# Performance work log

Hardware: AMD Instinct MI355X
Metric: run time of the kernel (lower is better)

## Reference

```python
import jax, jax.numpy as jnp
import numpy as np

# dims
B, LP, CIN, AUX = 8, 1024, 64, 32
COUT, OUT_LEN = 64, 512
DM, DI, NS, PH, NH = 1024, 2048, 16, 64, 32  # d_model, d_inner, d_state, headdim, n_heads
NL, PATCH, KPRE, KCONV = 4, 8, 5, 4
GG, KH, CHUNK = 8, 2048, 64  # kan grid, kan hidden, chunk_size
DIN = 2 * DI + 2 * NS + NH   # in_proj output: z, xBC, dt
CONV_DIM = DI + 2 * NS


def _conv1d(x, w, b, stride, pad_l, pad_r, groups=1):
    # x: [B, C, L], w: [O, I/groups, K]
    y = jax.lax.conv_general_dilated(x, w, (stride,), [(pad_l, pad_r)],
                                     dimension_numbers=("NCH", "OIH", "NCH"),
                                     feature_group_count=groups)
    return y + b[None, :, None]


def _rmsnorm(x, w):
    return x * jax.lax.rsqrt(jnp.mean(x * x, axis=-1, keepdims=True) + 1e-5) * w


def _mamba(u, in_w, conv_w, conv_b, A_log, Dh, dt_bias, out_w):
    # Mamba2-style selective SSM block (bias-free projections, causal depthwise conv).
    Bs, L, _ = u.shape
    zxbcdt = jnp.einsum("bld,ed->ble", u, in_w)  # [B,L,DIN]
    z = zxbcdt[..., :DI]
    xBC = zxbcdt[..., DI:DI + CONV_DIM]
    dt = jax.nn.softplus(zxbcdt[..., DI + CONV_DIM:] + dt_bias)  # [B,L,NH]
    xBC = jax.nn.silu(_conv1d(xBC.transpose(0, 2, 1), conv_w, conv_b, 1, KCONV - 1, 0,
                              groups=CONV_DIM)).transpose(0, 2, 1)
    xh = xBC[..., :DI].reshape(Bs, L, NH, PH)
    Bm = xBC[..., DI:DI + NS]   # [B,L,NS]
    Cm = xBC[..., DI + NS:]     # [B,L,NS]
    dA = jnp.exp(-jnp.exp(A_log) * dt)  # [B,L,NH]

    def step(s, t):
        x_t, B_t, C_t, dA_t, dt_t = t
        s = s * dA_t[:, :, None, None] + jnp.einsum("bhp,bn,bh->bhpn", x_t, B_t, dt_t)
        return s, jnp.einsum("bhpn,bn->bhp", s, C_t)

    s0 = jnp.zeros((Bs, NH, PH, NS), u.dtype)
    xs = (xh.transpose(1, 0, 2, 3), Bm.transpose(1, 0, 2), Cm.transpose(1, 0, 2),
          dA.transpose(1, 0, 2), dt.transpose(1, 0, 2))
    _, ys = jax.lax.scan(step, s0, xs)  # ys: [L,B,NH,PH]
    y = ys.transpose(1, 0, 2, 3) + xh * Dh[None, None, :, None]
    y = y.reshape(Bs, L, DI) * jax.nn.silu(z)
    return jnp.einsum("ble,de->bld", y, out_w)


def _kan(x, log_bw, base_w, base_b, spline_w):
    # Gaussian-basis KAN layer: base Linear + spline Linear over RBF expansion.
    grid = jnp.linspace(-2.0, 2.0, GG)
    bw = jnp.exp(log_bw)[None] + 1e-6                 # [1,in,1]
    basis = jnp.exp(-((x[..., None] - grid[None, None, :]) ** 2) / (2.0 * bw * bw))
    return x @ base_w.T + base_b + basis.reshape(x.shape[0], -1) @ spline_w.T


def setup_inputs() -> dict:
    ks = iter(jax.random.split(jax.random.key(0), 64))
    nrm = lambda shape, s=0.02: jax.random.normal(next(ks), shape, jnp.float32) * s
    inp = {"x_prefix": jax.random.normal(next(ks), (B, LP, CIN), jnp.float32),
           "y_aux": jax.random.normal(next(ks), (B, AUX), jnp.float32),
           "pre_conv_w": nrm((DM, CIN, KPRE), 0.1), "pre_conv_b": jnp.zeros((DM,)),
           "patch_w": nrm((DM, DM, PATCH), 0.05), "patch_b": jnp.zeros((DM,))}
    for pre in ("fwd", "bwd"):
        inp[pre + "_norm_w"] = jnp.ones((NL, DM))
        inp[pre + "_in_w"] = nrm((NL, DIN, DM))
        inp[pre + "_conv_w"] = nrm((NL, CONV_DIM, 1, KCONV), 0.1)
        inp[pre + "_conv_b"] = jnp.zeros((NL, CONV_DIM))
        inp[pre + "_A_log"] = jnp.zeros((NL, NH))
        inp[pre + "_D"] = jnp.ones((NL, NH))
        inp[pre + "_dt_bias"] = nrm((NL, NH), 0.5)
        inp[pre + "_out_w"] = nrm((NL, DM, DI))
    inp.update(aux_w=nrm((DM, AUX)), aux_b=jnp.zeros((DM,)),
               kan1_log_bw=jnp.zeros((3 * DM, 1)), kan1_base_w=nrm((KH, 3 * DM)),
               kan1_base_b=jnp.zeros((KH,)), kan1_spline_w=nrm((KH, 3 * DM * GG), 0.005),
               kan2_log_bw=jnp.zeros((KH, 1)), kan2_base_w=nrm((DM, KH)),
               kan2_base_b=jnp.zeros((DM,)), kan2_spline_w=nrm((DM, KH * GG), 0.005),
               shared_w=nrm((DM, DM)), shared_b=jnp.zeros((DM,)),
               heads_w=nrm((COUT, OUT_LEN, DM)), heads_b=jnp.zeros((COUT, OUT_LEN)))
    return inp


def reference(x_prefix, y_aux, pre_conv_w, pre_conv_b, patch_w, patch_b,
              fwd_norm_w, fwd_in_w, fwd_conv_w, fwd_conv_b, fwd_A_log, fwd_D, fwd_dt_bias, fwd_out_w,
              bwd_norm_w, bwd_in_w, bwd_conv_w, bwd_conv_b, bwd_A_log, bwd_D, bwd_dt_bias, bwd_out_w,
              aux_w, aux_b, kan1_log_bw, kan1_base_w, kan1_base_b, kan1_spline_w,
              kan2_log_bw, kan2_base_w, kan2_base_b, kan2_spline_w,
              shared_w, shared_b, heads_w, heads_b):
    # encode_prefix
    x = jax.nn.silu(_conv1d(x_prefix.transpose(0, 2, 1), pre_conv_w, pre_conv_b, 1, KPRE // 2, KPRE // 2))
    x = _conv1d(x, patch_w, patch_b, PATCH, 0, 0).transpose(0, 2, 1)  # [B, 128, DM]
    rem = x.shape[1] % CHUNK
    if rem:
        x = jnp.pad(x, ((0, 0), (0, CHUNK - rem), (0, 0)))
    h_f, h_b = x, x[:, ::-1]
    for i in range(NL):
        h_f = h_f + _mamba(_rmsnorm(h_f, fwd_norm_w[i]), fwd_in_w[i], fwd_conv_w[i], fwd_conv_b[i],
                           fwd_A_log[i], fwd_D[i], fwd_dt_bias[i], fwd_out_w[i])
        h_b = h_b + _mamba(_rmsnorm(h_b, bwd_norm_w[i]), bwd_in_w[i], bwd_conv_w[i], bwd_conv_b[i],
                           bwd_A_log[i], bwd_D[i], bwd_dt_bias[i], bwd_out_w[i])
    ctx = jnp.concatenate([h_f.mean(1), h_b[:, ::-1].mean(1)], axis=-1)  # [B, 2*DM]
    # fusion + heads
    aux = jax.nn.silu(y_aux @ aux_w.T + aux_b)
    fused = jnp.concatenate([ctx, aux], axis=-1)  # [B, 3*DM]
    fused = jax.nn.silu(_kan(fused, kan1_log_bw, kan1_base_w, kan1_base_b, kan1_spline_w))
    fused = jax.nn.silu(_kan(fused, kan2_log_bw, kan2_base_w, kan2_base_b, kan2_spline_w))
    fused = jax.nn.silu(fused @ shared_w.T + shared_b)
    # all channel heads fused into one batched GEMM: [B, OUT_LEN, COUT]
    return jnp.einsum("bd,cld->blc", fused, heads_w) + heads_b.T[None]
```

## Files before the change

### kernel.cpp

```cpp
#include <hip/hip_runtime.h>
#include <hip/hip_bf16.h>
#include <math.h>

#define B_    8
#define LP_   1024
#define CIN_  64
#define DM_   1024
#define DI_   2048
#define NS_   16
#define PH_   64
#define NH_   32
#define NL_   4
#define GG_   8
#define KH_   2048
#define DIN_  4160
#define NPAD_ 4224
#define CONVD_ 2080
#define L_    128
#define R_    1024
#define OUTL_ 512
#define COUT_ 64

typedef __bf16 bf16x8 __attribute__((ext_vector_type(8)));
typedef float f32x4 __attribute__((ext_vector_type(4)));
typedef unsigned short ushort;

__device__ __forceinline__ float silu_f(float x) { return x / (1.0f + expf(-x)); }

__device__ __forceinline__ ushort f2bu(float x) {
    union { __hip_bfloat16 h; ushort u; } c; c.h = __float2bfloat16(x); return c.u;
}
__device__ __forceinline__ float bu2f(ushort u) {
    union { ushort u; __hip_bfloat16 h; } c; c.u = u; return __bfloat162float(c.h);
}

__device__ __forceinline__ void gload_lds16(const void* g, void* l) {
    __builtin_amdgcn_global_load_lds((const __attribute__((address_space(1))) unsigned int*)g,
                                     (__attribute__((address_space(3))) unsigned int*)l, 16, 0, 0);
}

__device__ __forceinline__ float merge2(float a, float b, int mask, int lane) {
    float x = (lane & mask) ? b : a;
    float y = (lane & mask) ? a : b;
    return x + __shfl_xor(y, mask);
}
__device__ __forceinline__ float reduce8(float* a, int lane) {
    float c0 = merge2(a[0], a[1], 1, lane);
    float c1 = merge2(a[2], a[3], 1, lane);
    float c2 = merge2(a[4], a[5], 1, lane);
    float c3 = merge2(a[6], a[7], 1, lane);
    float d0 = merge2(c0, c1, 2, lane);
    float d1 = merge2(c2, c3, 2, lane);
    float e  = merge2(d0, d1, 4, lane);
    e += __shfl_xor(e, 8);
    e += __shfl_xor(e, 16);
    e += __shfl_xor(e, 32);
    return e;
}

__global__ __launch_bounds__(256) void k_pre_im2col(const float* __restrict__ xp, __hip_bfloat16* __restrict__ out) {
    size_t idx = (size_t)blockIdx.x * 256 + threadIdx.x;
    if (idx >= (size_t)8192 * 320) return;
    int kk = (int)(idx % 320); size_t r = idx / 320;
    int l = (int)(r & 1023); int b = (int)(r >> 10);
    int kp = kk >> 6, c = kk & 63;
    int lp = l + kp - 2;
    float v = 0.f;
    if (lp >= 0 && lp < LP_) v = xp[((size_t)b * LP_ + lp) * CIN_ + c];
    out[idx] = __float2bfloat16(v);
}

__global__ __launch_bounds__(256) void k_wpre_T(const float* __restrict__ w, __hip_bfloat16* __restrict__ out) {
    int idx = blockIdx.x * 256 + threadIdx.x;
    if (idx >= DM_ * 320) return;
    int d = idx / 320, kk = idx % 320;
    int kp = kk >> 6, c = kk & 63;
    out[idx] = __float2bfloat16(w[(d * CIN_ + c) * 5 + kp]);
}

__global__ __launch_bounds__(256) void k_wpatch_T(const float* __restrict__ w, __hip_bfloat16* __restrict__ out) {
    size_t idx = (size_t)blockIdx.x * 256 + threadIdx.x;
    if (idx >= (size_t)DM_ * 8192) return;
    int d = (int)(idx >> 13); int kk = (int)(idx & 8191);
    int kp = kk >> 10, din = kk & 1023;
    out[idx] = __float2bfloat16(w[((size_t)d << 13) + din * 8 + kp]);
}

#define CVT_IN_T4  1081344
#define CVT_OUT_T4 524288
__global__ __launch_bounds__(256) void k_cvt_layer(const float* __restrict__ in0, const float* __restrict__ in1,
                                                   const float* __restrict__ o0, const float* __restrict__ o1,
                                                   __hip_bfloat16* __restrict__ wBB, __hip_bfloat16* __restrict__ wOB) {
    int i = blockIdx.x * 256 + threadIdx.x;
    int dir = 0;
    if (i >= CVT_IN_T4 + CVT_OUT_T4) { dir = 1; i -= CVT_IN_T4 + CVT_OUT_T4; }
    const float* inw = dir ? in1 : in0;
    const float* outw = dir ? o1 : o0;
    if (i < CVT_IN_T4) {
        int idx = i * 4; int row = idx >> 10;
        __hip_bfloat16* dst = wBB + (size_t)dir * NPAD_ * 1024 + idx;
        if (row < DIN_) {
            float4 v = *(const float4*)(inw + idx);
            dst[0] = __float2bfloat16(v.x); dst[1] = __float2bfloat16(v.y);
            dst[2] = __float2bfloat16(v.z); dst[3] = __float2bfloat16(v.w);
        } else {
            dst[0] = __float2bfloat16(0.f); dst[1] = __float2bfloat16(0.f);
            dst[2] = __float2bfloat16(0.f); dst[3] = __float2bfloat16(0.f);
        }
    } else {
        int idx = (i - CVT_IN_T4) * 4;
        __hip_bfloat16* dst = wOB + (size_t)dir * 1024 * 2048 + idx;
        float4 v = *(const float4*)(outw + idx);
        dst[0] = __float2bfloat16(v.x); dst[1] = __float2bfloat16(v.y);
        dst[2] = __float2bfloat16(v.z); dst[3] = __float2bfloat16(v.w);
    }
}

template<int BM, int BN>
__global__ __launch_bounds__(256) void k_gemm_mfma(
    const ushort* __restrict__ A, const ushort* __restrict__ B,
    const float* __restrict__ bias,
    float* __restrict__ Cf, __hip_bfloat16* __restrict__ Cb,
    int Kc, int ldk, int ldc, int Nstore, int act, int nsplit,
    long sA, long sB, long sC)
{
    constexpr int BK = 32;
    constexpr int WM = BM / 2, WN = BN / 2;
    constexpr int MR = WM / 16, NR = WN / 16;
    constexpr int ACH = BM * 4, BCH = BN * 4;
    __shared__ ushort sAs[2][BM * BK];
    __shared__ ushort sBs[2][BN * BK];
    int tid = threadIdx.x;
    int lane = tid & 63, w = tid >> 6;
    int wr = w >> 1, wc = w & 1;
    int z = blockIdx.z;
    int dir = z / nsplit, ks = z - dir * nsplit;
    int kbase = ks * Kc;
    int m0 = blockIdx.y * BM, n0 = blockIdx.x * BN;
    const ushort* Az = A + (size_t)dir * sA + kbase;
    const ushort* Bz = B + (size_t)dir * sB + kbase;

    auto STAGE = [&](int buf, int k0) {
        #pragma unroll
        for (int c = tid; c < ACH; c += 256) {
            int row = c >> 2, col = (c & 3) * 8;
            gload_lds16(Az + (size_t)(m0 + row) * ldk + k0 + col, (char*)&sAs[buf][0] + c * 16);
        }
        #pragma unroll
        for (int c = tid; c < BCH; c += 256) {
            int row = c >> 2, col = (c & 3) * 8;
            gload_lds16(Bz + (size_t)(n0 + row) * ldk + k0 + col, (char*)&sBs[buf][0] + c * 16);
        }
    };

    f32x4 acc[MR][NR] = {};
    const int NT = Kc / BK;
    STAGE(0, 0);
    __syncthreads();
    int cur = 0;
    for (int t = 0; t < NT; ++t) {
        if (t + 1 < NT) STAGE(cur ^ 1, (t + 1) * BK);
        bf16x8 af[MR], bfr[NR];
        #pragma unroll
        for (int m = 0; m < MR; ++m)
            af[m] = *(const bf16x8*)&sAs[cur][(wr * WM + m * 16 + (lane & 15)) * BK + (lane >> 4) * 8];
        #pragma unroll
        for (int n = 0; n < NR; ++n)
            bfr[n] = *(const bf16x8*)&sBs[cur][(wc * WN + n * 16 + (lane & 15)) * BK + (lane >> 4) * 8];
        #pragma unroll
        for (int m = 0; m < MR; ++m)
            #pragma unroll
            for (int n = 0; n < NR; ++n)
                acc[m][n] = __builtin_amdgcn_mfma_f32_16x16x32_bf16(af[m], bfr[n], acc[m][n], 0, 0, 0);
        __syncthreads();
        cur ^= 1;
    }
    #pragma unroll
    for (int m = 0; m < MR; ++m) {
        int row = m0 + wr * WM + m * 16 + (lane >> 4) * 4;
        #pragma unroll
        for (int n = 0; n < NR; ++n) {
            int col = n0 + wc * WN + n * 16 + (lane & 15);
            if (col < Nstore) {
                if (act == 2) {
                    float* Cfz = Cf + (size_t)z * sC;
                    #pragma unroll
                    for (int j = 0; j < 4; ++j)
                        Cfz[(size_t)(row + j) * ldc + col] = acc[m][n][j];
                } else {
                    __hip_bfloat16* Cbz = Cb + (size_t)dir * sC;
                    float bv = bias ? bias[col] : 0.f;
                    #pragma unroll
                    for (int j = 0; j < 4; ++j) {
                        float v = acc[m][n][j] + bv;
                        if (act == 1) v = silu_f(v);
                        Cbz[(size_t)(row + j) * ldc + col] = __float2bfloat16(v);
                    }
                }
            }
        }
    }
}

__global__ __launch_bounds__(256) void k_patch_fin(const float* __restrict__ part, const float* __restrict__ bias,
                                                   float* __restrict__ hf, float* __restrict__ hb) {
    int i4 = blockIdx.x * 256 + threadIdx.x;
    int idx = i4 * 4;
    int r = idx >> 10, c = idx & 1023;
    float4 bv = *(const float4*)(bias + c);
    float4 o = bv;
    #pragma unroll
    for (int s = 0; s < 8; ++s) {
        float4 v = *(const float4*)(part + (size_t)s * 1048576 + idx);
        o.x += v.x; o.y += v.y; o.z += v.z; o.w += v.w;
    }
    *(float4*)(hf + idx) = o;
    *(float4*)(hb + (((size_t)(r ^ 127)) << 10) + c) = o;
}

__global__ __launch_bounds__(256) void k_oproj_fin(const float* __restrict__ part, float* __restrict__ h) {
    int i4 = blockIdx.x * 256 + threadIdx.x;
    int idx = i4 * 4;
    int dir = idx >> 20;
    int off = idx & 1048575;
    const float* p = part + (size_t)dir * 4 * 1048576 + off;
    float4 o = *(const float4*)(h + idx);
    #pragma unroll
    for (int s = 0; s < 4; ++s) {
        float4 v = *(const float4*)(p + (size_t)s * 1048576);
        o.x += v.x; o.y += v.y; o.z += v.z; o.w += v.w;
    }
    *(float4*)(h + idx) = o;
}

__global__ __launch_bounds__(256) void k_rmsnorm(const float* __restrict__ h, const float* __restrict__ w0,
                                                 const float* __restrict__ w1, __hip_bfloat16* __restrict__ u) {
    int r = blockIdx.x; int t = threadIdx.x;
    const float* w = (r >> 10) ? w1 : w0;
    const float* row = h + (size_t)r * DM_;
    float v[4]; float ss = 0.f;
    #pragma unroll
    for (int i = 0; i < 4; ++i) { v[i] = row[t + 256 * i]; ss += v[i] * v[i]; }
    #pragma unroll
    for (int o = 32; o; o >>= 1) ss += __shfl_xor(ss, o);
    __shared__ float sred[4];
    if ((t & 63) == 0) sred[t >> 6] = ss;
    __syncthreads();
    float tot = sred[0] + sred[1] + sred[2] + sred[3];
    float scale = rsqrtf(tot * (1.0f / DM_) + 1e-5f);
    #pragma unroll
    for (int i = 0; i < 4; ++i)
        u[(size_t)r * DM_ + t + 256 * i] = __float2bfloat16(v[i] * scale * w[t + 256 * i]);
}

__global__ __launch_bounds__(256) void k_scan(const __hip_bfloat16* __restrict__ zx,
                                              const float* __restrict__ cw0, const float* __restrict__ cw1,
                                              const float* __restrict__ cb0, const float* __restrict__ cb1,
                                              const float* __restrict__ dtb0, const float* __restrict__ dtb1,
                                              const float* __restrict__ al0, const float* __restrict__ al1,
                                              const float* __restrict__ D0, const float* __restrict__ D1,
                                              __hip_bfloat16* __restrict__ ys) {
    __shared__ float xs[L_ * PH_];
    __shared__ float Bsh[L_ * NS_];
    __shared__ float Csh[L_ * NS_];
    __shared__ float dts[L_];
    __shared__ float dAs[L_];
    int bx = blockIdx.x;
    int dir = bx >> 8, b = (bx >> 5) & 7, h = bx & 31;
    const __hip_bfloat16* zxd = zx + (size_t)dir * 1024 * DIN_;
    const float* cw = dir ? cw1 : cw0;
    const float* cb = dir ? cb1 : cb0;
    const float* dt_bias = dir ? dtb1 : dtb0;
    const float* A_log   = dir ? al1 : al0;
    const float* Dh      = dir ? D1 : D0;
    __hip_bfloat16* ysd  = ys + (size_t)dir * 1024 * DI_;
    int t = threadIdx.x;
    for (int i = t; i < 2048; i += 256) {
        int l = i >> 4, p4 = i & 15;
        int cc = h * PH_ + p4 * 4;
        float a0 = cb[cc + 0], a1 = cb[cc + 1], a2 = cb[cc + 2], a3 = cb[cc + 3];
        #pragma unroll
        for (int k = 0; k < 4; ++k) {
            int lp = l - 3 + k;
            if (lp >= 0) {
                ushort4 raw = *(const ushort4*)(zxd + (size_t)(b * L_ + lp) * DIN_ + DI_ + cc);
                a0 += bu2f(raw.x) * cw[(cc + 0) * 4 + k];
                a1 += bu2f(raw.y) * cw[(cc + 1) * 4 + k];
                a2 += bu2f(raw.z) * cw[(cc + 2) * 4 + k];
                a3 += bu2f(raw.w) * cw[(cc + 3) * 4 + k];
            }
        }
        float* xp = &xs[l * PH_ + p4 * 4];
        xp[0] = silu_f(a0); xp[1] = silu_f(a1); xp[2] = silu_f(a2); xp[3] = silu_f(a3);
    }
    for (int i = t; i < 1024; i += 256) {
        int l = i >> 3, q4 = i & 7;
        int cc = DI_ + q4 * 4;
        float a0 = cb[cc + 0], a1 = cb[cc + 1], a2 = cb[cc + 2], a3 = cb[cc + 3];
        #pragma unroll
        for (int k = 0; k < 4; ++k) {
            int lp = l - 3 + k;
            if (lp >= 0) {
                ushort4 raw = *(const ushort4*)(zxd + (size_t)(b * L_ + lp) * DIN_ + DI_ + cc);
                a0 += bu2f(raw.x) * cw[(cc + 0) * 4 + k];
                a1 += bu2f(raw.y) * cw[(cc + 1) * 4 + k];
                a2 += bu2f(raw.z) * cw[(cc + 2) * 4 + k];
                a3 += bu2f(raw.w) * cw[(cc + 3) * 4 + k];
            }
        }
        float r0 = silu_f(a0), r1 = silu_f(a1), r2 = silu_f(a2), r3 = silu_f(a3);
        if (q4 < 4) {
            float* bp = &Bsh[l * NS_ + q4 * 4];
            bp[0] = r0; bp[1] = r1; bp[2] = r2; bp[3] = r3;
        } else {
            float* cp = &Csh[l * NS_ + (q4 - 4) * 4];
            cp[0] = r0; cp[1] = r1; cp[2] = r2; cp[3] = r3;
        }
    }
    if (t < L_) {
        float v = bu2f(*(const ushort*)(zxd + (size_t)(b * L_ + t) * DIN_ + 4128 + h)) + dt_bias[h];
        float sp = v > 20.f ? v : log1pf(expf(v));
        dts[t] = sp;
        dAs[t] = expf(-expf(A_log[h]) * sp);
    }
    __syncthreads();
    int p = t >> 2, n0 = (t & 3) * 4;
    float Dv = Dh[h];
    float s0 = 0.f, s1 = 0.f, s2 = 0.f, s3 = 0.f;
    for (int l = 0; l < L_; ++l) {
        float x = xs[l * 64 + p];
        float dAv = dAs[l];
        float xdt = x * dts[l];
        s0 = s0 * dAv + xdt * Bsh[l * 16 + n0 + 0];
        s1 = s1 * dAv + xdt * Bsh[l * 16 + n0 + 1];
        s2 = s2 * dAv + xdt * Bsh[l * 16 + n0 + 2];
        s3 = s3 * dAv + xdt * Bsh[l * 16 + n0 + 3];
        float cp = s0 * Csh[l * 16 + n0 + 0] + s1 * Csh[l * 16 + n0 + 1]
                 + s2 * Csh[l * 16 + n0 + 2] + s3 * Csh[l * 16 + n0 + 3];
        cp += __shfl_xor(cp, 1);
        cp += __shfl_xor(cp, 2);
        if ((t & 3) == 0) xs[l * 64 + p] = cp + x * Dv;
    }
    __syncthreads();
    for (int i = t; i < L_ * PH_; i += 256) {
        int l = i >> 6, pp = i & 63;
        float z = bu2f(*(const ushort*)(zxd + (size_t)(b * L_ + l) * DIN_ + h * PH_ + pp));
        ysd[((size_t)(b * L_ + l)) * DI_ + h * PH_ + pp] = __float2bfloat16(xs[i] * silu_f(z));
    }
}

__global__ __launch_bounds__(256) void k_meanctx(const float* __restrict__ hf, const float* __restrict__ hb,
                                                 float* __restrict__ fused) {
    int b = blockIdx.x >> 3, ch = blockIdx.x & 7;
    int t = threadIdx.x;
    int d4 = t & 31, lg = t >> 5;
    int d = ch * 128 + d4 * 4;
    float4 sf = {0,0,0,0}, sb = {0,0,0,0};
    for (int l = lg; l < L_; l += 8) {
        float4 a = *(const float4*)(hf + ((size_t)b * L_ + l) * DM_ + d);
        float4 c = *(const float4*)(hb + ((size_t)b * L_ + l) * DM_ + d);
        sf.x += a.x; sf.y += a.y; sf.z += a.z; sf.w += a.w;
        sb.x += c.x; sb.y += c.y; sb.z += c.z; sb.w += c.w;
    }
    __shared__ float rf[8][128], rb[8][128];
    *(float4*)&rf[lg][d4 * 4] = sf;
    *(float4*)&rb[lg][d4 * 4] = sb;
    __syncthreads();
    if (t < 128) {
        float s1 = 0.f, s2 = 0.f;
        #pragma unroll
        for (int g = 0; g < 8; ++g) { s1 += rf[g][t]; s2 += rb[g][t]; }
        fused[b * 3072 + ch * 128 + t] = s1 * (1.f / L_);
        fused[b * 3072 + DM_ + ch * 128 + t] = s2 * (1.f / L_);
    }
}

__global__ __launch_bounds__(256) void k_aux(const float* __restrict__ y_aux, const float* __restrict__ aux_w,
                                             const float* __restrict__ aux_b, float* __restrict__ fused) {
    int j = blockIdx.x * 256 + threadIdx.x;
    if (j >= DM_) return;
    for (int b = 0; b < B_; ++b) {
        float acc = aux_b[j];
        for (int a = 0; a < 32; ++a) acc += y_aux[b * 32 + a] * aux_w[j * 32 + a];
        fused[b * 3072 + 2 * DM_ + j] = silu_f(acc);
    }
}

__global__ __launch_bounds__(256) void k_basis(const float* __restrict__ x, const float* __restrict__ log_bw,
                                               float* __restrict__ basis, int Din) {
    int idx = blockIdx.x * 256 + threadIdx.x;
    if (idx >= 8 * Din) return;
    int d = idx % Din;
    float xv = x[idx];
    float bw = expf(log_bw[d]) + 1e-6f;
    float inv = 1.0f / (2.0f * bw * bw);
    #pragma unroll
    for (int g = 0; g < GG_; ++g) {
        float gg = -2.0f + g * (4.0f / 7.0f);
        float df = xv - gg;
        basis[(size_t)idx * GG_ + g] = expf(-df * df * inv);
    }
}

template<int MODE>
__global__ __launch_bounds__(256) void k_dotl(const float* __restrict__ W, const float* __restrict__ X,
                                              const float* __restrict__ bias, float* __restrict__ out,
                                              int K, int Dout, int ldx, int nch, int chOff) {
    __shared__ float sX[8][1024];
    int ch = blockIdx.y;
    int k0 = ch * 1024;
    int tid = threadIdx.x;
    for (int i = tid; i < 2048; i += 256) {
        int b = i >> 8, kk = (i & 255) * 4;
        *(float4*)&sX[b][kk] = *(const float4*)(X + (size_t)b * ldx + k0 + kk);
    }
    __syncthreads();
    int wv = tid >> 6, lane = tid & 63;
    int rowBase = blockIdx.x * 32 + wv * 8;
    for (int j = 0; j < 8; ++j) {
        int row = rowBase + j;
        const float* wr = W + (size_t)row * K + k0;
        float acc[8] = {};
        #pragma unroll
        for (int it = 0; it < 4; ++it) {
            int k = it * 256 + lane * 4;
            float4 wvv = *(const float4*)(wr + k);
            #pragma unroll
            for (int b = 0; b < 8; ++b) {
                float4 xv = *(const float4*)&sX[b][k];
                acc[b] += wvv.x * xv.x + wvv.y * xv.y + wvv.z * xv.z + wvv.w * xv.w;
            }
        }
        float e = reduce8(acc, lane);
        if (lane < 8) {
            if (MODE == 0) {
                out[((size_t)row * nch + chOff + ch) * 8 + lane] = e;
            } else if (MODE == 1) {
                out[(size_t)lane * Dout + row] = silu_f(e + bias[row]);
            } else {
                int c = row >> 9, l = row & 511;
                out[((size_t)lane * OUTL_ + l) * COUT_ + c] = e + bias[row];
            }
        }
    }
}

template<int NCH>
__global__ __launch_bounds__(256) void k_dot_fin(const float* __restrict__ partial, const float* __restrict__ base_b,
                                                 float* __restrict__ out, int Dout) {
    int row = blockIdx.x * 256 + threadIdx.x;
    if (row >= Dout) return;
    float bb = base_b[row];
    #pragma unroll
    for (int b = 0; b < 8; ++b) {
        float s = bb;
        #pragma unroll
        for (int c = 0; c < NCH; ++c) s += partial[((size_t)row * NCH + c) * 8 + b];
        out[(size_t)b * Dout + row] = silu_f(s);
    }
}

extern "C" void kernel_launch(void* const* d_in, const int* in_sizes, int n_in,
                              void* d_out, int out_size, void* d_ws, size_t ws_size,
                              hipStream_t stream) {
    const float* x_prefix = (const float*)d_in[0];
    const float* y_aux    = (const float*)d_in[1];
    const float* pre_w    = (const float*)d_in[2];
    const float* pre_b    = (const float*)d_in[3];
    const float* patch_w  = (const float*)d_in[4];
    const float* patch_b  = (const float*)d_in[5];
    const float* norm_w[2] = {(const float*)d_in[6],  (const float*)d_in[14]};
    const float* in_w[2]   = {(const float*)d_in[7],  (const float*)d_in[15]};
    const float* conv_w[2] = {(const float*)d_in[8],  (const float*)d_in[16]};
    const float* conv_b[2] = {(const float*)d_in[9],  (const float*)d_in[17]};
    const float* A_log[2]  = {(const float*)d_in[10], (const float*)d_in[18]};
    const float* Dvec[2]   = {(const float*)d_in[11], (const float*)d_in[19]};
    const float* dt_b[2]   = {(const float*)d_in[12], (const float*)d_in[20]};
    const float* out_w[2]  = {(const float*)d_in[13], (const float*)d_in[21]};
    const float* aux_w = (const float*)d_in[22];
    const float* aux_b = (const float*)d_in[23];
    const float* k1_lbw = (const float*)d_in[24];
    const float* k1_bw  = (const float*)d_in[25];
    const float* k1_bb  = (const float*)d_in[26];
    const float* k1_sw  = (const float*)d_in[27];
    const float* k2_lbw = (const float*)d_in[28];
    const float* k2_bw  = (const float*)d_in[29];
    const float* k2_bb  = (const float*)d_in[30];
    const float* k2_sw  = (const float*)d_in[31];
    const float* sh_w = (const float*)d_in[32];
    const float* sh_b = (const float*)d_in[33];
    const float* hw   = (const float*)d_in[34];
    const float* hbias= (const float*)d_in[35];
    float* ws = (float*)d_ws;
    float* out = (float*)d_out;

    const size_t o_ApreB   = 0;
    const size_t o_wpreTB  = 1310720;
    const size_t o_x1B     = 1474560;
    const size_t o_wpatchTB= 5668864;
    const size_t o_uB   = 0;
    const size_t o_zxB  = 1048576;
    const size_t o_ysB  = 5308416;
    const size_t o_wBB  = 7405568;
    const size_t o_wOB  = 11730944;
    const size_t o_hf   = 13828096;
    const size_t o_hb   = 14876672;
    const size_t o_spart= 15925248;
    const size_t total_f = 24313856;
    const size_t o_f1   = 0;
    const size_t o_bas1 = 24576;
    const size_t o_k1   = 221184;
    const size_t o_bas2 = 237568;
    const size_t o_k2   = 368640;
    const size_t o_f4   = 376832;
    const size_t o_part = 385024;
    if (ws_size < total_f * sizeof(float)) return;

    __hip_bfloat16* ApreB   = (__hip_bfloat16*)(ws + o_ApreB);
    __hip_bfloat16* wpreTB  = (__hip_bfloat16*)(ws + o_wpreTB);
    __hip_bfloat16* x1B     = (__hip_bfloat16*)(ws + o_x1B);
    __hip_bfloat16* wpatchTB= (__hip_bfloat16*)(ws + o_wpatchTB);
    __hip_bfloat16* uB      = (__hip_bfloat16*)(ws + o_uB);
    __hip_bfloat16* zxB     = (__hip_bfloat16*)(ws + o_zxB);
    __hip_bfloat16* ysB     = (__hip_bfloat16*)(ws + o_ysB);
    __hip_bfloat16* wBB     = (__hip_bfloat16*)(ws + o_wBB);
    __hip_bfloat16* wOB     = (__hip_bfloat16*)(ws + o_wOB);
    float* hf = ws + o_hf;
    float* hb = ws + o_hb;

    k_wpre_T<<<1280, 256, 0, stream>>>(pre_w, wpreTB);
    k_wpatch_T<<<32768, 256, 0, stream>>>(patch_w, wpatchTB);
    k_pre_im2col<<<10240, 256, 0, stream>>>(x_prefix, ApreB);
    k_gemm_mfma<128,128><<<dim3(8, 64, 1), 256, 0, stream>>>(
        (const ushort*)ApreB, (const ushort*)wpreTB, pre_b, nullptr, x1B,
        320, 320, 1024, 1024, 1, 1, 0, 0, 0);
    k_gemm_mfma<128,128><<<dim3(8, 8, 8), 256, 0, stream>>>(
        (const ushort*)x1B, (const ushort*)wpatchTB, nullptr, ws + o_spart, nullptr,
        1024, 8192, 1024, 1024, 2, 8, 0, 0, (long)1024 * 1024);
    k_patch_fin<<<1024, 256, 0, stream>>>(ws + o_spart, patch_b, hf, hb);

    for (int i = 0; i < NL_; ++i) {
        k_rmsnorm<<<2048, 256, 0, stream>>>(hf, norm_w[0] + (size_t)i * DM_, norm_w[1] + (size_t)i * DM_, uB);
        k_cvt_layer<<<12544, 256, 0, stream>>>(
            in_w[0] + (size_t)i * DIN_ * DM_, in_w[1] + (size_t)i * DIN_ * DM_,
            out_w[0] + (size_t)i * DM_ * DI_, out_w[1] + (size_t)i * DM_ * DI_, wBB, wOB);
        k_gemm_mfma<128,128><<<dim3(33, 8, 2), 256, 0, stream>>>(
            (const ushort*)uB, (const ushort*)wBB, nullptr, nullptr, zxB,
            1024, 1024, DIN_, DIN_, 0, 1, (long)1024 * 1024, (long)NPAD_ * 1024, (long)1024 * DIN_);
        k_scan<<<512, 256, 0, stream>>>(zxB,
            conv_w[0] + (size_t)i * CONVD_ * 4, conv_w[1] + (size_t)i * CONVD_ * 4,
            conv_b[0] + (size_t)i * CONVD_, conv_b[1] + (size_t)i * CONVD_,
            dt_b[0] + i * NH_, dt_b[1] + i * NH_, A_log[0] + i * NH_, A_log[1] + i * NH_,
            Dvec[0] + i * NH_, Dvec[1] + i * NH_, ysB);
        k_gemm_mfma<128,128><<<dim3(8, 8, 8), 256, 0, stream>>>(
            (const ushort*)ysB, (const ushort*)wOB, nullptr, ws + o_spart, nullptr,
            512, 2048, 1024, 1024, 2, 4, (long)1024 * 2048, (long)1024 * 2048, (long)1024 * 1024);
        k_oproj_fin<<<2048, 256, 0, stream>>>(ws + o_spart, hf);
    }

    k_meanctx<<<64, 256, 0, stream>>>(hf, hb, ws + o_f1);
    k_aux<<<4, 256, 0, stream>>>(y_aux, aux_w, aux_b, ws + o_f1);
    k_basis<<<96, 256, 0, stream>>>(ws + o_f1, k1_lbw, ws + o_bas1, 3072);
    k_dotl<0><<<dim3(64, 24), 256, 0, stream>>>(k1_sw, ws + o_bas1, nullptr, ws + o_part, 24576, 2048, 24576, 27, 0);
    k_dotl<0><<<dim3(64, 3),  256, 0, stream>>>(k1_bw, ws + o_f1,   nullptr, ws + o_part, 3072,  2048, 3072,  27, 24);
    k_dot_fin<27><<<8, 256, 0, stream>>>(ws + o_part, k1_bb, ws + o_k1, 2048);
    k_basis<<<64, 256, 0, stream>>>(ws + o_k1, k2_lbw, ws + o_bas2, 2048);
    k_dotl<0><<<dim3(32, 16), 256, 0, stream>>>(k2_sw, ws + o_bas2, nullptr, ws + o_part, 16384, 1024, 16384, 18, 0);
    k_dotl<0><<<dim3(32, 2),  256, 0, stream>>>(k2_bw, ws + o_k1,   nullptr, ws + o_part, 2048,  1024, 2048,  18, 16);
    k_dot_fin<18><<<4, 256, 0, stream>>>(ws + o_part, k2_bb, ws + o_k2, 1024);
    k_dotl<1><<<dim3(32, 1), 256, 0, stream>>>(sh_w, ws + o_k2, sh_b, ws + o_f4, 1024, 1024, 1024, 1, 0);
    k_dotl<2><<<dim3(1024, 1), 256, 0, stream>>>(hw, ws + o_f4, hbias, out, 1024, 32768, 1024, 1, 0);
}
```

Before: 918.7 us.

## Fuse small kernels and convert all layer weights up front in one launch

Merges the three preprocessing kernels into one launch, and converts all layers' weights to bf16 in a single kernel before the layer loop instead of once per layer. The residual-add finish kernels now also compute the next layer's RMSNorm, and the mean/aux, KAN spline/base dot, and finish+basis kernels are merged. The aim is to cut kernel launch count and extra passes over the activations, at the cost of a much larger workspace holding all converted weights.

Measured after the change: 883.0 us. -3.9%, faster.

```diff
diff --git a/kernel.cpp b/kernel.cpp
--- a/kernel.cpp
+++ b/kernel.cpp
@@ -58,47 +58,51 @@
     return e;
 }
 
-__global__ __launch_bounds__(256) void k_pre_im2col(const float* __restrict__ xp, __hip_bfloat16* __restrict__ out) {
-    size_t idx = (size_t)blockIdx.x * 256 + threadIdx.x;
-    if (idx >= (size_t)8192 * 320) return;
-    int kk = (int)(idx % 320); size_t r = idx / 320;
-    int l = (int)(r & 1023); int b = (int)(r >> 10);
-    int kp = kk >> 6, c = kk & 63;
-    int lp = l + kp - 2;
-    float v = 0.f;
-    if (lp >= 0 && lp < LP_) v = xp[((size_t)b * LP_ + lp) * CIN_ + c];
-    out[idx] = __float2bfloat16(v);
-}
-
-__global__ __launch_bounds__(256) void k_wpre_T(const float* __restrict__ w, __hip_bfloat16* __restrict__ out) {
+#define PREP_W1 327680
+#define PREP_W2 8388608
+#define PREP_W3 2621440
+__global__ __launch_bounds__(256) void k_prep(const float* __restrict__ pre_w, const float* __restrict__ patch_w,
+                                              const float* __restrict__ xp,
+                                              __hip_bfloat16* __restrict__ wpreT, __hip_bfloat16* __restrict__ wpatchT,
+                                              __hip_bfloat16* __restrict__ Apre) {
     int idx = blockIdx.x * 256 + threadIdx.x;
-    if (idx >= DM_ * 320) return;
-    int d = idx / 320, kk = idx % 320;
-    int kp = kk >> 6, c = kk & 63;
-    out[idx] = __float2bfloat16(w[(d * CIN_ + c) * 5 + kp]);
-}
-
-__global__ __launch_bounds__(256) void k_wpatch_T(const float* __restrict__ w, __hip_bfloat16* __restrict__ out) {
-    size_t idx = (size_t)blockIdx.x * 256 + threadIdx.x;
-    if (idx >= (size_t)DM_ * 8192) return;
-    int d = (int)(idx >> 13); int kk = (int)(idx & 8191);
-    int kp = kk >> 10, din = kk & 1023;
-    out[idx] = __float2bfloat16(w[((size_t)d << 13) + din * 8 + kp]);
+    if (idx < PREP_W1) {
+        int d = idx / 320, kk = idx % 320;
+        int kp = kk >> 6, c = kk & 63;
+        wpreT[idx] = __float2bfloat16(pre_w[(d * CIN_ + c) * 5 + kp]);
+    } else if (idx < PREP_W1 + PREP_W2) {
+        int i = idx - PREP_W1;
+        int d = i >> 13, kk = i & 8191;
+        int kp = kk >> 10, din = kk & 1023;
+        wpatchT[i] = __float2bfloat16(patch_w[((size_t)d << 13) + din * 8 + kp]);
+    } else if (idx < PREP_W1 + PREP_W2 + PREP_W3) {
+        int i = idx - PREP_W1 - PREP_W2;
+        int kk = i % 320; int r = i / 320;
+        int l = r & 1023, b = r >> 10;
+        int kp = kk >> 6, c = kk & 63;
+        int lp = l + kp - 2;
+        float v = 0.f;
+        if (lp >= 0 && lp < LP_) v = xp[((size_t)b * LP_ + lp) * CIN_ + c];
+        Apre[i] = __float2bfloat16(v);
+    }
 }
 
 #define CVT_IN_T4  1081344
 #define CVT_OUT_T4 524288
-__global__ __launch_bounds__(256) void k_cvt_layer(const float* __restrict__ in0, const float* __restrict__ in1,
-                                                   const float* __restrict__ o0, const float* __restrict__ o1,
-                                                   __hip_bfloat16* __restrict__ wBB, __hip_bfloat16* __restrict__ wOB) {
+#define CVT_PER    1605632
+__global__ __launch_bounds__(256) void k_cvt_all(const float* __restrict__ in0, const float* __restrict__ in1,
+                                                 const float* __restrict__ o0, const float* __restrict__ o1,
+                                                 __hip_bfloat16* __restrict__ wBBa, __hip_bfloat16* __restrict__ wOBa) {
     int i = blockIdx.x * 256 + threadIdx.x;
-    int dir = 0;
-    if (i >= CVT_IN_T4 + CVT_OUT_T4) { dir = 1; i -= CVT_IN_T4 + CVT_OUT_T4; }
-    const float* inw = dir ? in1 : in0;
-    const float* outw = dir ? o1 : o0;
-    if (i < CVT_IN_T4) {
-        int idx = i * 4; int row = idx >> 10;
-        __hip_bfloat16* dst = wBB + (size_t)dir * NPAD_ * 1024 + idx;
+    if (i >= 8 * CVT_PER) return;
+    int ld = i / CVT_PER;
+    int r = i - ld * CVT_PER;
+    int l = ld >> 1, d = ld & 1;
+    const float* inw  = (d ? in1 : in0) + (size_t)l * DIN_ * DM_;
+    const float* outw = (d ? o1 : o0) + (size_t)l * DM_ * DI_;
+    if (r < CVT_IN_T4) {
+        int idx = r * 4; int row = idx >> 10;
+        __hip_bfloat16* dst = wBBa + (size_t)ld * NPAD_ * 1024 + idx;
         if (row < DIN_) {
             float4 v = *(const float4*)(inw + idx);
             dst[0] = __float2bfloat16(v.x); dst[1] = __float2bfloat16(v.y);
@@ -108,8 +112,8 @@
             dst[2] = __float2bfloat16(0.f); dst[3] = __float2bfloat16(0.f);
         }
     } else {
-        int idx = (i - CVT_IN_T4) * 4;
-        __hip_bfloat16* dst = wOB + (size_t)dir * 1024 * 2048 + idx;
+        int idx = (r - CVT_IN_T4) * 4;
+        __hip_bfloat16* dst = wOBa + (size_t)ld * 2048 * 1024 + idx;
         float4 v = *(const float4*)(outw + idx);
         dst[0] = __float2bfloat16(v.x); dst[1] = __float2bfloat16(v.y);
         dst[2] = __float2bfloat16(v.z); dst[3] = __float2bfloat16(v.w);
@@ -202,55 +206,70 @@
     }
 }
 
-__global__ __launch_bounds__(256) void k_patch_fin(const float* __restrict__ part, const float* __restrict__ bias,
-                                                   float* __restrict__ hf, float* __restrict__ hb) {
-    int i4 = blockIdx.x * 256 + threadIdx.x;
-    int idx = i4 * 4;
-    int r = idx >> 10, c = idx & 1023;
-    float4 bv = *(const float4*)(bias + c);
-    float4 o = bv;
+__global__ __launch_bounds__(256) void k_patch_fin_rms(const float* __restrict__ part, const float* __restrict__ bias,
+                                                       const float* __restrict__ w0, const float* __restrict__ w1,
+                                                       float* __restrict__ hf, float* __restrict__ hb,
+                                                       __hip_bfloat16* __restrict__ uB) {
+    int r = blockIdx.x;
+    int t = threadIdx.x;
+    int c = t * 4;
+    float4 o = *(const float4*)(bias + c);
     #pragma unroll
     for (int s = 0; s < 8; ++s) {
-        float4 v = *(const float4*)(part + (size_t)s * 1048576 + idx);
+        float4 v = *(const float4*)(part + (size_t)s * 1048576 + ((size_t)r << 10) + c);
         o.x += v.x; o.y += v.y; o.z += v.z; o.w += v.w;
     }
-    *(float4*)(hf + idx) = o;
-    *(float4*)(hb + (((size_t)(r ^ 127)) << 10) + c) = o;
-}
-
-__global__ __launch_bounds__(256) void k_oproj_fin(const float* __restrict__ part, float* __restrict__ h) {
-    int i4 = blockIdx.x * 256 + threadIdx.x;
-    int idx = i4 * 4;
-    int dir = idx >> 20;
-    int off = idx & 1048575;
-    const float* p = part + (size_t)dir * 4 * 1048576 + off;
-    float4 o = *(const float4*)(h + idx);
+    *(float4*)(hf + ((size_t)r << 10) + c) = o;
+    int rb = r ^ 127;
+    *(float4*)(hb + ((size_t)rb << 10) + c) = o;
+    float ss = o.x * o.x + o.y * o.y + o.z * o.z + o.w * o.w;
     #pragma unroll
-    for (int s = 0; s < 4; ++s) {
-        float4 v = *(const float4*)(p + (size_t)s * 1048576);
-        o.x += v.x; o.y += v.y; o.z += v.z; o.w += v.w;
-    }
-    *(float4*)(h + idx) = o;
-}
-
-__global__ __launch_bounds__(256) void k_rmsnorm(const float* __restrict__ h, const float* __restrict__ w0,
-                                                 const float* __restrict__ w1, __hip_bfloat16* __restrict__ u) {
-    int r = blockIdx.x; int t = threadIdx.x;
-    const float* w = (r >> 10) ? w1 : w0;
-    const float* row = h + (size_t)r * DM_;
-    float v[4]; float ss = 0.f;
-    #pragma unroll
-    for (int i = 0; i < 4; ++i) { v[i] = row[t + 256 * i]; ss += v[i] * v[i]; }
-    #pragma unroll
-    for (int o = 32; o; o >>= 1) ss += __shfl_xor(ss, o);
+    for (int of = 32; of; of >>= 1) ss += __shfl_xor(ss, of);
     __shared__ float sred[4];
     if ((t & 63) == 0) sred[t >> 6] = ss;
     __syncthreads();
     float tot = sred[0] + sred[1] + sred[2] + sred[3];
     float scale = rsqrtf(tot * (1.0f / DM_) + 1e-5f);
+    float4 wf = *(const float4*)(w0 + c);
+    float4 wb = *(const float4*)(w1 + c);
+    __hip_bfloat16* uf = uB + ((size_t)r << 10) + c;
+    __hip_bfloat16* ub = uB + ((size_t)(1024 + rb) << 10) + c;
+    uf[0] = __float2bfloat16(o.x * scale * wf.x); uf[1] = __float2bfloat16(o.y * scale * wf.y);
+    uf[2] = __float2bfloat16(o.z * scale * wf.z); uf[3] = __float2bfloat16(o.w * scale * wf.w);
+    ub[0] = __float2bfloat16(o.x * scale * wb.x); ub[1] = __float2bfloat16(o.y * scale * wb.y);
+    ub[2] = __float2bfloat16(o.z * scale * wb.z); ub[3] = __float2bfloat16(o.w * scale * wb.w);
+}
+
+template<bool DO_RMS>
+__global__ __launch_bounds__(256) void k_oproj_fin_rms(const float* __restrict__ part,
+                                                       const float* __restrict__ w0, const float* __restrict__ w1,
+                                                       float* __restrict__ h, __hip_bfloat16* __restrict__ uB) {
+    int row = blockIdx.x;
+    int t = threadIdx.x;
+    int c = t * 4;
+    const float* p = part + (size_t)(row >> 10) * 4194304 + (size_t)(row & 1023) * 1024 + c;
+    float4 o = *(const float4*)(h + ((size_t)row << 10) + c);
     #pragma unroll
-    for (int i = 0; i < 4; ++i)
-        u[(size_t)r * DM_ + t + 256 * i] = __float2bfloat16(v[i] * scale * w[t + 256 * i]);
+    for (int s = 0; s < 4; ++s) {
+        float4 v = *(const float4*)(p + (size_t)s * 1048576);
+        o.x += v.x; o.y += v.y; o.z += v.z; o.w += v.w;
+    }
+    *(float4*)(h + ((size_t)row << 10) + c) = o;
+    if (DO_RMS) {
+        float ss = o.x * o.x + o.y * o.y + o.z * o.z + o.w * o.w;
+        #pragma unroll
+        for (int of = 32; of; of >>= 1) ss += __shfl_xor(ss, of);
+        __shared__ float sred[4];
+        if ((t & 63) == 0) sred[t >> 6] = ss;
+        __syncthreads();
+        float tot = sred[0] + sred[1] + sred[2] + sred[3];
+        float scale = rsqrtf(tot * (1.0f / DM_) + 1e-5f);
+        const float* w = (row >> 10) ? w1 : w0;
+        float4 wv = *(const float4*)(w + c);
+        __hip_bfloat16* u = uB + ((size_t)row << 10) + c;
+        u[0] = __float2bfloat16(o.x * scale * wv.x); u[1] = __float2bfloat16(o.y * scale * wv.y);
+        u[2] = __float2bfloat16(o.z * scale * wv.z); u[3] = __float2bfloat16(o.w * scale * wv.w);
+    }
 }
 
 __global__ __launch_bounds__(256) void k_scan(const __hip_bfloat16* __restrict__ zx,
@@ -349,40 +368,41 @@
     }
 }
 
-__global__ __launch_bounds__(256) void k_meanctx(const float* __restrict__ hf, const float* __restrict__ hb,
-                                                 float* __restrict__ fused) {
-    int b = blockIdx.x >> 3, ch = blockIdx.x & 7;
+__global__ __launch_bounds__(256) void k_meanctx_aux(const float* __restrict__ hf, const float* __restrict__ hb,
+                                                     const float* __restrict__ y_aux, const float* __restrict__ aux_w,
+                                                     const float* __restrict__ aux_b, float* __restrict__ fused) {
+    int bx = blockIdx.x;
     int t = threadIdx.x;
-    int d4 = t & 31, lg = t >> 5;
-    int d = ch * 128 + d4 * 4;
-    float4 sf = {0,0,0,0}, sb = {0,0,0,0};
-    for (int l = lg; l < L_; l += 8) {
-        float4 a = *(const float4*)(hf + ((size_t)b * L_ + l) * DM_ + d);
-        float4 c = *(const float4*)(hb + ((size_t)b * L_ + l) * DM_ + d);
-        sf.x += a.x; sf.y += a.y; sf.z += a.z; sf.w += a.w;
-        sb.x += c.x; sb.y += c.y; sb.z += c.z; sb.w += c.w;
-    }
-    __shared__ float rf[8][128], rb[8][128];
-    *(float4*)&rf[lg][d4 * 4] = sf;
-    *(float4*)&rb[lg][d4 * 4] = sb;
-    __syncthreads();
-    if (t < 128) {
-        float s1 = 0.f, s2 = 0.f;
-        #pragma unroll
-        for (int g = 0; g < 8; ++g) { s1 += rf[g][t]; s2 += rb[g][t]; }
-        fused[b * 3072 + ch * 128 + t] = s1 * (1.f / L_);
-        fused[b * 3072 + DM_ + ch * 128 + t] = s2 * (1.f / L_);
-    }
-}
-
-__global__ __launch_bounds__(256) void k_aux(const float* __restrict__ y_aux, const float* __restrict__ aux_w,
-                                             const float* __restrict__ aux_b, float* __restrict__ fused) {
-    int j = blockIdx.x * 256 + threadIdx.x;
-    if (j >= DM_) return;
-    for (int b = 0; b < B_; ++b) {
-        float acc = aux_b[j];
-        for (int a = 0; a < 32; ++a) acc += y_aux[b * 32 + a] * aux_w[j * 32 + a];
-        fused[b * 3072 + 2 * DM_ + j] = silu_f(acc);
+    if (bx < 64) {
+        int b = bx >> 3, ch = bx & 7;
+        int d4 = t & 31, lg = t >> 5;
+        int d = ch * 128 + d4 * 4;
+        float4 sf = {0,0,0,0}, sb = {0,0,0,0};
+        for (int l = lg; l < L_; l += 8) {
+            float4 a = *(const float4*)(hf + ((size_t)b * L_ + l) * DM_ + d);
+            float4 c = *(const float4*)(hb + ((size_t)b * L_ + l) * DM_ + d);
+            sf.x += a.x; sf.y += a.y; sf.z += a.z; sf.w += a.w;
+            sb.x += c.x; sb.y += c.y; sb.z += c.z; sb.w += c.w;
+        }
+        __shared__ float rf[8][128], rb[8][128];
+        *(float4*)&rf[lg][d4 * 4] = sf;
+        *(float4*)&rb[lg][d4 * 4] = sb;
+        __syncthreads();
+        if (t < 128) {
+            float s1 = 0.f, s2 = 0.f;
+            #pragma unroll
+            for (int g = 0; g < 8; ++g) { s1 += rf[g][t]; s2 += rb[g][t]; }
+            fused[b * 3072 + ch * 128 + t] = s1 * (1.f / L_);
+            fused[b * 3072 + DM_ + ch * 128 + t] = s2 * (1.f / L_);
+        }
+    } else {
+        int j = (bx - 64) * 256 + t;
+        if (j >= DM_) return;
+        for (int b = 0; b < B_; ++b) {
+            float acc = aux_b[j];
+            for (int a = 0; a < 32; ++a) acc += y_aux[b * 32 + a] * aux_w[j * 32 + a];
+            fused[b * 3072 + 2 * DM_ + j] = silu_f(acc);
+        }
     }
 }
 
@@ -403,16 +423,21 @@
 }
 
 template<int MODE>
-__global__ __launch_bounds__(256) void k_dotl(const float* __restrict__ W, const float* __restrict__ X,
+__global__ __launch_bounds__(256) void k_dotk(const float* __restrict__ Wsp, const float* __restrict__ Xsp, int Ksp,
+                                              const float* __restrict__ Wb, const float* __restrict__ Xb, int Kb,
                                               const float* __restrict__ bias, float* __restrict__ out,
-                                              int K, int Dout, int ldx, int nch, int chOff) {
+                                              int nsp, int nch, int Dout) {
     __shared__ float sX[8][1024];
     int ch = blockIdx.y;
-    int k0 = ch * 1024;
+    bool sp = (ch < nsp);
+    const float* W = sp ? Wsp : Wb;
+    const float* X = sp ? Xsp : Xb;
+    int K = sp ? Ksp : Kb;
+    int k0 = (sp ? ch : ch - nsp) * 1024;
     int tid = threadIdx.x;
     for (int i = tid; i < 2048; i += 256) {
         int b = i >> 8, kk = (i & 255) * 4;
-        *(float4*)&sX[b][kk] = *(const float4*)(X + (size_t)b * ldx + k0 + kk);
+        *(float4*)&sX[b][kk] = *(const float4*)(X + (size_t)b * K + k0 + kk);
     }
     __syncthreads();
     int wv = tid >> 6, lane = tid & 63;
@@ -434,13 +459,37 @@
         float e = reduce8(acc, lane);
         if (lane < 8) {
             if (MODE == 0) {
-                out[((size_t)row * nch + chOff + ch) * 8 + lane] = e;
+                out[((size_t)row * nch + ch) * 8 + lane] = e;
             } else if (MODE == 1) {
                 out[(size_t)lane * Dout + row] = silu_f(e + bias[row]);
             } else {
                 int c = row >> 9, l = row & 511;
                 out[((size_t)lane * OUTL_ + l) * COUT_ + c] = e + bias[row];
             }
+        }
+    }
+}
+
+__global__ __launch_bounds__(256) void k_fin1_basis2(const float* __restrict__ partial, const float* __restrict__ bb,
+                                                     const float* __restrict__ k2_lbw,
+                                                     float* __restrict__ k1, float* __restrict__ bas2) {
+    int row = blockIdx.x * 256 + threadIdx.x;
+    if (row >= 2048) return;
+    float bbv = bb[row];
+    float lb = expf(k2_lbw[row]) + 1e-6f;
+    float inv = 1.0f / (2.0f * lb * lb);
+    #pragma unroll
+    for (int b = 0; b < 8; ++b) {
+        float s = bbv;
+        #pragma unroll
+        for (int c = 0; c < 27; ++c) s += partial[((size_t)row * 27 + c) * 8 + b];
+        float v = silu_f(s);
+        k1[(size_t)b * 2048 + row] = v;
+        #pragma unroll
+        for (int g = 0; g < GG_; ++g) {
+            float gg = -2.0f + g * (4.0f / 7.0f);
+            float df = v - gg;
+            bas2[((size_t)b * 2048 + row) * GG_ + g] = expf(-df * df * inv);
         }
     }
 }
@@ -501,12 +550,12 @@
     const size_t o_uB   = 0;
     const size_t o_zxB  = 1048576;
     const size_t o_ysB  = 5308416;
-    const size_t o_wBB  = 7405568;
-    const size_t o_wOB  = 11730944;
-    const size_t o_hf   = 13828096;
-    const size_t o_hb   = 14876672;
-    const size_t o_spart= 15925248;
-    const size_t total_f = 24313856;
+    const size_t o_hf   = 9863168;
+    const size_t o_hb   = 10911744;
+    const size_t o_wBBa = 11960320;
+    const size_t o_wOBa = 29261824;
+    const size_t o_spart= 37650432;
+    const size_t total_f = 46039040;
     const size_t o_f1   = 0;
     const size_t o_bas1 = 24576;
     const size_t o_k1   = 221184;
@@ -523,29 +572,24 @@
     __hip_bfloat16* uB      = (__hip_bfloat16*)(ws + o_uB);
     __hip_bfloat16* zxB     = (__hip_bfloat16*)(ws + o_zxB);
     __hip_bfloat16* ysB     = (__hip_bfloat16*)(ws + o_ysB);
-    __hip_bfloat16* wBB     = (__hip_bfloat16*)(ws + o_wBB);
-    __hip_bfloat16* wOB     = (__hip_bfloat16*)(ws + o_wOB);
+    __hip_bfloat16* wBBa    = (__hip_bfloat16*)(ws + o_wBBa);
+    __hip_bfloat16* wOBa    = (__hip_bfloat16*)(ws + o_wOBa);
     float* hf = ws + o_hf;
     float* hb = ws + o_hb;
 
-    k_wpre_T<<<1280, 256, 0, stream>>>(pre_w, wpreTB);
-    k_wpatch_T<<<32768, 256, 0, stream>>>(patch_w, wpatchTB);
-    k_pre_im2col<<<10240, 256, 0, stream>>>(x_prefix, ApreB);
+    k_cvt_all<<<50176, 256, 0, stream>>>(in_w[0], in_w[1], out_w[0], out_w[1], wBBa, wOBa);
+    k_prep<<<44288, 256, 0, stream>>>(pre_w, patch_w, x_prefix, wpreTB, wpatchTB, ApreB);
     k_gemm_mfma<128,128><<<dim3(8, 64, 1), 256, 0, stream>>>(
         (const ushort*)ApreB, (const ushort*)wpreTB, pre_b, nullptr, x1B,
         320, 320, 1024, 1024, 1, 1, 0, 0, 0);
     k_gemm_mfma<128,128><<<dim3(8, 8, 8), 256, 0, stream>>>(
         (const ushort*)x1B, (const ushort*)wpatchTB, nullptr, ws + o_spart, nullptr,
         1024, 8192, 1024, 1024, 2, 8, 0, 0, (long)1024 * 1024);
-    k_patch_fin<<<1024, 256, 0, stream>>>(ws + o_spart, patch_b, hf, hb);
+    k_patch_fin_rms<<<1024, 256, 0, stream>>>(ws + o_spart, patch_b, norm_w[0], norm_w[1], hf, hb, uB);
 
     for (int i = 0; i < NL_; ++i) {
-        k_rmsnorm<<<2048, 256, 0, stream>>>(hf, norm_w[0] + (size_t)i * DM_, norm_w[1] + (size_t)i * DM_, uB);
-        k_cvt_layer<<<12544, 256, 0, stream>>>(
-            in_w[0] + (size_t)i * DIN_ * DM_, in_w[1] + (size_t)i * DIN_ * DM_,
-            out_w[0] + (size_t)i * DM_ * DI_, out_w[1] + (size_t)i * DM_ * DI_, wBB, wOB);
         k_gemm_mfma<128,128><<<dim3(33, 8, 2), 256, 0, stream>>>(
-            (const ushort*)uB, (const ushort*)wBB, nullptr, nullptr, zxB,
+            (const ushort*)uB, (const ushort*)(wBBa + (size_t)i * 2 * NPAD_ * 1024), nullptr, nullptr, zxB,
             1024, 1024, DIN_, DIN_, 0, 1, (long)1024 * 1024, (long)NPAD_ * 1024, (long)1024 * DIN_);
         k_scan<<<512, 256, 0, stream>>>(zxB,
             conv_w[0] + (size_t)i * CONVD_ * 4, conv_w[1] + (size_t)i * CONVD_ * 4,
@@ -553,21 +597,26 @@
             dt_b[0] + i * NH_, dt_b[1] + i * NH_, A_log[0] + i * NH_, A_log[1] + i * NH_,
             Dvec[0] + i * NH_, Dvec[1] + i * NH_, ysB);
         k_gemm_mfma<128,128><<<dim3(8, 8, 8), 256, 0, stream>>>(
-            (const ushort*)ysB, (const ushort*)wOB, nullptr, ws + o_spart, nullptr,
-            512, 2048, 1024, 1024, 2, 4, (long)1024 * 2048, (long)1024 * 2048, (long)1024 * 1024);
-        k_oproj_fin<<<2048, 256, 0, stream>>>(ws + o_spart, hf);
-    }
-
-    k_meanctx<<<64, 256, 0, stream>>>(hf, hb, ws + o_f1);
-    k_aux<<<4, 256, 0, stream>>>(y_aux, aux_w, aux_b, ws + o_f1);
+            (const ushort*)ysB, (const ushort*)(wOBa + (size_t)i * 2 * 2048 * 1024), nullptr, ws + o_spart, nullptr,
+            512, 2048, 1024, 1024, 2, 4, (long)1024 * 2048, (long)2048 * 1024, (long)1024 * 1024);
+        if (i + 1 < NL_) {
+            k_oproj_fin_rms<true><<<2048, 256, 0, stream>>>(ws + o_spart,
+                norm_w[0] + (size_t)(i + 1) * DM_, norm_w[1] + (size_t)(i + 1) * DM_, hf, uB);
+        } else {
+            k_oproj_fin_rms<false><<<2048, 256, 0, stream>>>(ws + o_spart, nullptr, nullptr, hf, nullptr);
+        }
+    }
+
+    k_meanctx_aux<<<68, 256, 0, stream>>>(hf, hb, y_aux, aux_w, aux_b, ws + o_f1);
     k_basis<<<96, 256, 0, stream>>>(ws + o_f1, k1_lbw, ws + o_bas1, 3072);
-    k_dotl<0><<<dim3(64, 24), 256, 0, stream>>>(k1_sw, ws + o_bas1, nullptr, ws + o_part, 24576, 2048, 24576, 27, 0);
-    k_dotl<0><<<dim3(64, 3),  256, 0, stream>>>(k1_bw, ws + o_f1,   nullptr, ws + o_part, 3072,  2048, 3072,  27, 24);
-    k_dot_fin<27><<<8, 256, 0, stream>>>(ws + o_part, k1_bb, ws + o_k1, 2048);
-    k_basis<<<64, 256, 0, stream>>>(ws + o_k1, k2_lbw, ws + o_bas2, 2048);
-    k_dotl<0><<<dim3(32, 16), 256, 0, stream>>>(k2_sw, ws + o_bas2, nullptr, ws + o_part, 16384, 1024, 16384, 18, 0);
-    k_dotl<0><<<dim3(32, 2),  256, 0, stream>>>(k2_bw, ws + o_k1,   nullptr, ws + o_part, 2048,  1024, 2048,  18, 16);
+    k_dotk<0><<<dim3(64, 27), 256, 0, stream>>>(k1_sw, ws + o_bas1, 24576, k1_bw, ws + o_f1, 3072,
+                                                nullptr, ws + o_part, 24, 27, 2048);
+    k_fin1_basis2<<<8, 256, 0, stream>>>(ws + o_part, k1_bb, k2_lbw, ws + o_k1, ws + o_bas2);
+    k_dotk<0><<<dim3(32, 18), 256, 0, stream>>>(k2_sw, ws + o_bas2, 16384, k2_bw, ws + o_k1, 2048,
+                                                nullptr, ws + o_part, 16, 18, 1024);
     k_dot_fin<18><<<4, 256, 0, stream>>>(ws + o_part, k2_bb, ws + o_k2, 1024);
-    k_dotl<1><<<dim3(32, 1), 256, 0, stream>>>(sh_w, ws + o_k2, sh_b, ws + o_f4, 1024, 1024, 1024, 1, 0);
-    k_dotl<2><<<dim3(1024, 1), 256, 0, stream>>>(hw, ws + o_f4, hbias, out, 1024, 32768, 1024, 1, 0);
-}
+    k_dotk<1><<<dim3(32, 1), 256, 0, stream>>>(nullptr, nullptr, 0, sh_w, ws + o_k2, 1024,
+                                               sh_b, ws + o_f4, 0, 1, 1024);
+    k_dotk<2><<<dim3(1024, 1), 256, 0, stream>>>(nullptr, nullptr, 0, hw, ws + o_f4, 1024,
+                                                 hbias, out, 0, 1, 32768);
+}
```
